# Kernel tuning notes

Hardware: AMD Instinct MI355X
Metric: run time of the kernel (lower is better)

Reference implementation:

```python
import jax, jax.numpy as jnp
import numpy as np

KAPPA = 1.0
SIGMA = 0.3
EPS = 1e-5  # torch BatchNorm1d default eps


def _bn(y, g, b):
    # training-mode batch norm: biased batch statistics over the batch axis
    mu = jnp.mean(y, axis=0)
    var = jnp.mean((y - mu) ** 2, axis=0)
    return g * (y - mu) * jax.lax.rsqrt(var + EPS) + b


def _hid(x, W, b, g, be):
    # Linear -> BatchNorm1d -> ReLU
    return jax.nn.relu(_bn(x @ W + b, g, be))


def setup_inputs() -> dict:
    key = jax.random.key(0)
    ks = jax.random.split(key, 12)
    B, D, H, T = 2048, 256, 266, 51  # H = dim + 10
    S = T - 1
    sc = jnp.float32(0.1)
    f32 = jnp.float32
    inp = {}
    inp["x"] = jax.random.normal(ks[0], (B, D), f32)
    inp["dW"] = jax.random.normal(ks[1], (S, B, D), f32)   # hoisted per-step noise xi
    inp["law"] = jax.random.normal(ks[2], (S, D), f32)
    inp["timegrid"] = jnp.linspace(0.0, 1.0, T).astype(f32)
    # per-timestep MLP stacks (i_h1 / h1_h2 / h2_o)
    inp["W1"] = sc * jax.random.normal(ks[3], (S, D, H), f32)
    inp["b1"] = jnp.zeros((S, H), f32)
    inp["g1"] = jnp.ones((S, H), f32)
    inp["be1"] = jnp.zeros((S, H), f32)
    inp["W2"] = sc * jax.random.normal(ks[4], (S, H, H), f32)
    inp["b2"] = jnp.zeros((S, H), f32)
    inp["g2"] = jnp.ones((S, H), f32)
    inp["be2"] = jnp.zeros((S, H), f32)
    inp["W3"] = sc * jax.random.normal(ks[5], (S, H, D), f32)
    inp["b3"] = jnp.zeros((S, D), f32)
    # v0 network (v0_i_h1 / v0_h1_h2 / v0_h2_o, all Linear+BN+ReLU)
    inp["Wv1"] = sc * jax.random.normal(ks[6], (D, H), f32)
    inp["bv1"] = jnp.zeros((H,), f32)
    inp["gv1"] = jnp.ones((H,), f32)
    inp["bev1"] = jnp.zeros((H,), f32)
    inp["Wv2"] = sc * jax.random.normal(ks[7], (H, H), f32)
    inp["bv2"] = jnp.zeros((H,), f32)
    inp["gv2"] = jnp.ones((H,), f32)
    inp["bev2"] = jnp.zeros((H,), f32)
    inp["Wv3"] = sc * jax.random.normal(ks[8], (H, 1), f32)
    inp["bv3"] = jnp.zeros((1,), f32)
    inp["gv3"] = jnp.ones((1,), f32)
    inp["bev3"] = jnp.zeros((1,), f32)
    return inp


def reference(x, dW, law, timegrid,
              W1, b1, g1, be1, W2, b2, g2, be2, W3, b3,
              Wv1, bv1, gv1, bev1, Wv2, bv2, gv2, bev2, Wv3, bv3, gv3, bev3):
    hgrid = jnp.diff(timegrid)  # [S]
    # v0 network evaluated on the initial state (note: last stage is also Linear+BN+ReLU)
    v0 = _hid(_hid(_hid(x, Wv1, bv1, gv1, bev1), Wv2, bv2, gv2, bev2), Wv3, bv3, gv3, bev3)  # [B,1]

    def step(carry, xs):
        xc, v = carry
        w1, bb1, gg1, bbe1, w2, bb2, gg2, bbe2, w3, bb3, li, dw, h = xs
        h1 = _hid(xc, w1, bb1, gg1, bbe1)
        h2 = _hid(h1, w2, bb2, gg2, bbe2)
        grad = h2 @ w3 + bb3                                   # [B,D]
        # f = kappa^2/2 * ||x - law_i||^2 + 1/2 * ||alpha||^2,  alpha = -grad
        f = 0.5 * KAPPA ** 2 * jnp.sum((xc - li) ** 2, axis=1) + 0.5 * jnp.sum(grad ** 2, axis=1)
        noise = SIGMA * jnp.sqrt(h) * dw                       # [B,D]
        # diag(grad @ noise^T) == rowwise dot product: O(B*D) instead of O(B^2*D)
        v = v - (f * h)[:, None] + jnp.sum(grad * noise, axis=1, keepdims=True)
        xc = xc - grad * h + noise
        return (xc, v), None

    (x_final, v), _ = jax.lax.scan(
        step, (x, v0),
        (W1, b1, g1, be1, W2, b2, g2, be2, W3, b3, law, dW, hgrid))
    return v  # [B,1]; (x_final and the path are byproducts of the same scan)
```

## Files before the change

kernel.cpp:

```cpp
#include <hip/hip_runtime.h>
#include <hip/hip_bf16.h>


#define BATCH 2048
#define DD    256
#define HH    266
#define HP    272
#define SS    50
#define BN_EPS 1e-5f
#define SIG   0.3f
#define AS_STRIDE 296
#define YS    276
#define XS    260

#define V_OFF  1638400
#define S1_OFF 1640448
#define S2_OFF 1649152
#define S1V_OFF 1657856
#define S2V_OFF 1662208
#define SV_OFF  1666560
#define WQ_OFF  1666576

#define W1S 69632
#define W2S 78336
#define W3S 73728
#define W1Q_OFF 0
#define W2Q_OFF 3481600
#define W3Q_OFF 7398400
#define WV1Q_OFF 11084800
#define WV2Q_OFF 11154432

#define BAR_OFF 7283200

typedef unsigned short ushort_t;
using short8 = __attribute__((ext_vector_type(8))) short;
using f32x4  = __attribute__((ext_vector_type(4))) float;
using f32x2  = __attribute__((ext_vector_type(2))) float;

__device__ __forceinline__ ushort_t f2b(float f) {
    unsigned u = __float_as_uint(f);
    unsigned r = u + 0x7FFF + ((u >> 16) & 1);
    return (ushort_t)(r >> 16);
}

__device__ __forceinline__ float ld_coh(const float* p) {
    return __hip_atomic_load((const float*)p, __ATOMIC_RELAXED, __HIP_MEMORY_SCOPE_AGENT);
}
__device__ __forceinline__ f32x2 ld2_coh(const float* p) {
    f32x2 v;
    asm volatile("global_load_dwordx2 %0, %1, off sc0 sc1" : "=v"(v) : "v"(p));
    return v;
}
__device__ __forceinline__ void pf2(const f32x4* q, int n, int tid,
                                    f32x4& r0, f32x4& r1) {
    int i0 = (tid < n) ? tid : 0;
    int i1 = (tid + 512 < n) ? (tid + 512) : 0;
    r0 = q[i0];
    r1 = q[i1];
}

__global__ __launch_bounds__(256) void k_conv(const float* __restrict__ src,
                                              ushort_t* __restrict__ dst,
                                              int K, int N, int KT, int NT,
                                              long total) {
    long t = (long)blockIdx.x * 256 + threadIdx.x;
    if (t >= total) return;
    int per = KT * NT * 512;
    int step = (int)(t / per);
    int e = (int)(t - (long)step * per);
    int kt = e / (NT * 512);
    int r = e - kt * NT * 512;
    int nt = r / 512;
    int r2 = r & 511;
    int lane = r2 >> 3;
    int j = r2 & 7;
    int k = kt * 32 + (lane >> 4) * 8 + j;
    int n = nt * 16 + (lane & 15);
    float v = (k < K && n < N) ? src[(size_t)step * K * N + (size_t)k * N + n] : 0.f;
    dst[t] = f2b(v);
}

__global__ __launch_bounds__(256) void k_pre(float* __restrict__ ws) {
    unsigned* bar = (unsigned*)(ws + BAR_OFF);
    for (int i = threadIdx.x; i < 768; i += 256) atomicExch(bar + i, 0u);
}

__device__ __forceinline__ void grid_bar(unsigned* bar, unsigned gen, int bid) {
    __syncthreads();
    if (threadIdx.x == 0) {
        const int lf = bid & 7;
        unsigned* leaf = bar + lf * 32;
        unsigned* root = bar + 256;
        unsigned* rel  = bar + 288 + lf * 32;
        bool done = false;
        unsigned a = __hip_atomic_fetch_add(leaf, 1u, __ATOMIC_RELAXED, __HIP_MEMORY_SCOPE_AGENT);
        if (a == gen * 16u + 15u) {
            unsigned r = __hip_atomic_fetch_add(root, 1u, __ATOMIC_RELAXED, __HIP_MEMORY_SCOPE_AGENT);
            if (r == gen * 8u + 7u) {
                #pragma unroll
                for (int l = 0; l < 8; ++l)
                    __hip_atomic_store(bar + 288 + l * 32, gen + 1u, __ATOMIC_RELAXED, __HIP_MEMORY_SCOPE_AGENT);
                done = true;
            }
        }
        if (!done) {
            while (__hip_atomic_load(rel, __ATOMIC_RELAXED, __HIP_MEMORY_SCOPE_AGENT) < gen + 1u)
                __builtin_amdgcn_s_sleep(1);
        }
        asm volatile("" ::: "memory");
    }
    __syncthreads();
}

__device__ __forceinline__ void compute_ac_coh(const float* __restrict__ si,
                                               const float* __restrict__ g,
                                               const float* __restrict__ be,
                                               float (*AC)[HP]) {
    int t = threadIdx.x;
    if (t < 136) {
        f32x2 sv[8], qv[8];
        #pragma unroll
        for (int r = 0; r < 8; ++r) {
            sv[r] = ld2_coh(si + r * 544 + 2 * t);
            qv[r] = ld2_coh(si + r * 544 + 272 + 2 * t);
        }
        asm volatile("s_waitcnt vmcnt(0)" ::: "memory");
        __builtin_amdgcn_sched_barrier(0);
        f32x2 s = sv[0], q = qv[0];
        #pragma unroll
        for (int r = 1; r < 8; ++r) { s += sv[r]; q += qv[r]; }
        #pragma unroll
        for (int j = 0; j < 2; ++j) {
            int col = 2 * t + j;
            float a = 0.f, c = 0.f;
            if (col < HH) {
                float mu  = s[j] * (1.0f / 2048.0f);
                float var = q[j] * (1.0f / 2048.0f) - mu * mu;
                float rs  = rsqrtf(fmaxf(var, 0.0f) + BN_EPS);
                a = g[col] * rs;
                c = be[col] - mu * a;
            }
            AC[0][col] = a;
            AC[1][col] = c;
        }
    }
}

__device__ __forceinline__ void dev_lin16(
    int bid, int mode, int KT,
    const float* __restrict__ gsrc, const float* __restrict__ lsrc,
    const float* __restrict__ stats_in, const float* __restrict__ g,
    const float* __restrict__ be,
    const ushort_t* __restrict__ Wq, const float* __restrict__ bias,
    float* __restrict__ ylds, float* __restrict__ stats_out,
    float* __restrict__ zero_ptr,
    ushort_t* __restrict__ As, float (*AC)[HP])
{
    const int tid  = threadIdx.x;
    const int lane = tid & 63;
    const int wv   = tid >> 6;
    const int quad = lane >> 4;
    const int l15  = lane & 15;
    const int row0 = bid * 16;

    if (zero_ptr != nullptr && tid < 34)
        atomicExch(zero_ptr + bid * 34 + tid, 0.0f);

    if (mode == 2) { compute_ac_coh(stats_in, g, be, AC); __syncthreads(); }

    const int PAIRS = KT * 16;
    for (int idx = tid; idx < 16 * PAIRS; idx += 512) {
        int m  = idx / PAIRS;
        int kk = (idx - m * PAIRS) * 2;
        float v0, v1;
        if (mode == 2) {
            v0 = (kk < HH)   ? fmaxf(fmaf(AC[0][kk],   lsrc[m * YS + kk],   AC[1][kk]),   0.f) : 0.f;
            v1 = (kk+1 < HH) ? fmaxf(fmaf(AC[0][kk+1], lsrc[m * YS + kk+1], AC[1][kk+1]), 0.f) : 0.f;
        } else {
            v0 = gsrc[(size_t)(row0 + m) * DD + kk];
            v1 = gsrc[(size_t)(row0 + m) * DD + kk + 1];
        }
        ((unsigned int*)As)[m * (AS_STRIDE/2) + (kk >> 1)] =
            (unsigned int)f2b(v0) | ((unsigned int)f2b(v1) << 16);
    }
    __syncthreads();

    f32x4 acc[3];
    #pragma unroll
    for (int i = 0; i < 3; ++i) acc[i] = (f32x4){0.f, 0.f, 0.f, 0.f};

    #pragma unroll 3
    for (int kt = 0; kt < KT; ++kt) {
        short8 af = *(const short8*)(&As[l15 * AS_STRIDE + kt * 32 + quad * 8]);
        const ushort_t* wp = Wq + ((size_t)(kt * 17 + wv)) * 512 + lane * 8;
        #pragma unroll
        for (int i = 0; i < 3; ++i) {
            if (i < 2 || wv == 0) {
                short8 bf = *(const short8*)(wp + (size_t)i * 8 * 512);
                acc[i] = __builtin_amdgcn_mfma_f32_16x16x32_bf16(af, bf, acc[i], 0, 0, 0);
            }
        }
    }

    #pragma unroll
    for (int i = 0; i < 3; ++i) {
        if (i == 2 && wv != 0) continue;
        int t = wv + 8 * i;
        int col = t * 16 + l15;
        float bj = (col < HH) ? bias[col] : 0.f;
        float y0 = acc[i][0] + bj, y1 = acc[i][1] + bj;
        float y2 = acc[i][2] + bj, y3 = acc[i][3] + bj;
        ylds[(quad*4 + 0) * YS + col] = y0;
        ylds[(quad*4 + 1) * YS + col] = y1;
        ylds[(quad*4 + 2) * YS + col] = y2;
        ylds[(quad*4 + 3) * YS + col] = y3;
        float sp = y0 + y1 + y2 + y3;
        float sq = y0*y0 + y1*y1 + y2*y2 + y3*y3;
        sp += __shfl_xor(sp, 16); sp += __shfl_xor(sp, 32);
        sq += __shfl_xor(sq, 16); sq += __shfl_xor(sq, 32);
        if (quad == 0 && col < HH) {
            float* spp = stats_out + (bid & 7) * 544;
            atomicAdd(spp + col, sp);
            atomicAdd(spp + 272 + col, sq);
        }
    }
}

__device__ __forceinline__ void dev_fused16(
    int bid,
    const float* __restrict__ y2l, const float* __restrict__ stats_in,
    const float* __restrict__ g2, const float* __restrict__ be2,
    const ushort_t* __restrict__ W3q, const float* __restrict__ b3,
    const float* __restrict__ law, const float* __restrict__ dWs,
    const float* __restrict__ tg, int s, int doP1,
    float* __restrict__ xcl, float* __restrict__ vv, float* __restrict__ outv,
    const ushort_t* __restrict__ W1q, const float* __restrict__ b1n,
    float* __restrict__ y1l, float* __restrict__ stats_out,
    float* __restrict__ zero_ptr,
    ushort_t* __restrict__ As, float (*AC)[HP], float* __restrict__ red)
{
    const int tid  = threadIdx.x;
    const int lane = tid & 63;
    const int wv   = tid >> 6;
    const int quad = lane >> 4;
    const int l15  = lane & 15;
    const int row0 = bid * 16;

    if (zero_ptr != nullptr && tid < 34)
        atomicExch(zero_ptr + bid * 34 + tid, 0.0f);

    compute_ac_coh(stats_in, g2, be2, AC);
    __syncthreads();

    for (int idx = tid; idx < 16 * 144; idx += 512) {
        int m  = idx / 144;
        int kk = (idx - m * 144) * 2;
        float v0 = (kk < HH)   ? fmaxf(fmaf(AC[0][kk],   y2l[m * YS + kk],   AC[1][kk]),   0.f) : 0.f;
        float v1 = (kk+1 < HH) ? fmaxf(fmaf(AC[0][kk+1], y2l[m * YS + kk+1], AC[1][kk+1]), 0.f) : 0.f;
        ((unsigned int*)As)[m * (AS_STRIDE/2) + (kk >> 1)] =
            (unsigned int)f2b(v0) | ((unsigned int)f2b(v1) << 16);
    }
    __syncthreads();

    f32x4 acc[2];
    acc[0] = (f32x4){0.f,0.f,0.f,0.f};
    acc[1] = (f32x4){0.f,0.f,0.f,0.f};
    #pragma unroll 3
    for (int kt = 0; kt < 9; ++kt) {
        short8 af = *(const short8*)(&As[l15 * AS_STRIDE + kt * 32 + quad * 8]);
        const ushort_t* wp = W3q + ((size_t)(kt * 16 + wv)) * 512 + lane * 8;
        acc[0] = __builtin_amdgcn_mfma_f32_16x16x32_bf16(af, *(const short8*)(wp),           acc[0], 0, 0, 0);
        acc[1] = __builtin_amdgcn_mfma_f32_16x16x32_bf16(af, *(const short8*)(wp + 8 * 512), acc[1], 0, 0, 0);
    }

    const float h   = tg[s + 1] - tg[s];
    const float srt = SIG * sqrtf(h);
    float grad[2][4], xcv[2][4], dwv[2][4];
    float sxr[4], sgr[4], sgnr[4];
    #pragma unroll
    for (int i = 0; i < 2; ++i) {
        int col = (wv + 8*i) * 16 + l15;
        const float lawv = law[col];
        const float b3v  = b3[col];
        #pragma unroll
        for (int r = 0; r < 4; ++r) {
            int rl = quad * 4 + r;
            float gd = acc[i][r] + b3v;
            float xv = xcl[rl * XS + col];
            float dw = dWs[(size_t)(row0 + rl) * DD + col];
            float d  = xv - lawv;
            grad[i][r] = gd; xcv[i][r] = xv; dwv[i][r] = dw;
            if (i == 0) {
                sxr[r]  = d * d;
                sgr[r]  = gd * gd;
                sgnr[r] = gd * dw;
            } else {
                sxr[r]  = fmaf(d, d, sxr[r]);
                sgr[r]  = fmaf(gd, gd, sgr[r]);
                sgnr[r] = fmaf(gd, dw, sgnr[r]);
            }
        }
    }
    #pragma unroll
    for (int off = 1; off < 16; off <<= 1) {
        #pragma unroll
        for (int r = 0; r < 4; ++r) {
            sxr[r]  += __shfl_xor(sxr[r],  off);
            sgr[r]  += __shfl_xor(sgr[r],  off);
            sgnr[r] += __shfl_xor(sgnr[r], off);
        }
    }
    if (l15 == 0) {
        #pragma unroll
        for (int r = 0; r < 4; ++r) {
            int rr = quad * 4 + r;
            red[(wv * 16 + rr) * 3 + 0] = sxr[r];
            red[(wv * 16 + rr) * 3 + 1] = sgr[r];
            red[(wv * 16 + rr) * 3 + 2] = sgnr[r];
        }
    }
    __syncthreads();

    if (tid < 16) {
        float sx = 0.f, sg = 0.f, sgn = 0.f;
        #pragma unroll
        for (int w = 0; w < 8; ++w) {
            sx  += red[(w * 16 + tid) * 3 + 0];
            sg  += red[(w * 16 + tid) * 3 + 1];
            sgn += red[(w * 16 + tid) * 3 + 2];
        }
        int row = row0 + tid;
        float f  = 0.5f * (sx + sg);
        float vn = vv[row] - f * h + srt * sgn;
        vv[row] = vn;
        if (s == SS - 1) outv[row] = vn;
    }

    #pragma unroll
    for (int i = 0; i < 2; ++i) {
        int col = (wv + 8*i) * 16 + l15;
        #pragma unroll
        for (int r = 0; r < 4; ++r) {
            int rl = quad * 4 + r;
            float xn = xcv[i][r] - grad[i][r] * h + srt * dwv[i][r];
            xcl[rl * XS + col] = xn;
            if (doP1) As[rl * AS_STRIDE + col] = f2b(xn);
        }
    }
    if (!doP1) return;
    __syncthreads();

    f32x4 acc2[3];
    #pragma unroll
    for (int i = 0; i < 3; ++i) acc2[i] = (f32x4){0.f, 0.f, 0.f, 0.f};
    #pragma unroll 4
    for (int kt = 0; kt < 8; ++kt) {
        short8 af = *(const short8*)(&As[l15 * AS_STRIDE + kt * 32 + quad * 8]);
        const ushort_t* wp = W1q + ((size_t)(kt * 17 + wv)) * 512 + lane * 8;
        #pragma unroll
        for (int i = 0; i < 3; ++i) {
            if (i < 2 || wv == 0) {
                short8 bf = *(const short8*)(wp + (size_t)i * 8 * 512);
                acc2[i] = __builtin_amdgcn_mfma_f32_16x16x32_bf16(af, bf, acc2[i], 0, 0, 0);
            }
        }
    }
    #pragma unroll
    for (int i = 0; i < 3; ++i) {
        if (i == 2 && wv != 0) continue;
        int t = wv + 8 * i;
        int col = t * 16 + l15;
        float bj = (col < HH) ? b1n[col] : 0.f;
        float y0 = acc2[i][0] + bj, y1 = acc2[i][1] + bj;
        float y2 = acc2[i][2] + bj, y3 = acc2[i][3] + bj;
        y1l[(quad*4 + 0) * YS + col] = y0;
        y1l[(quad*4 + 1) * YS + col] = y1;
        y1l[(quad*4 + 2) * YS + col] = y2;
        y1l[(quad*4 + 3) * YS + col] = y3;
        float sp = y0 + y1 + y2 + y3;
        float sq = y0*y0 + y1*y1 + y2*y2 + y3*y3;
        sp += __shfl_xor(sp, 16); sp += __shfl_xor(sp, 32);
        sq += __shfl_xor(sq, 16); sq += __shfl_xor(sq, 32);
        if (quad == 0 && col < HH) {
            float* spp = stats_out + (bid & 7) * 544;
            atomicAdd(spp + col, sp);
            atomicAdd(spp + 272 + col, sq);
        }
    }
}

__device__ __forceinline__ void dev_v0l3_16(
    int bid, const float* __restrict__ y2l, const float* __restrict__ stats_in,
    const float* __restrict__ gv, const float* __restrict__ bev,
    const float* __restrict__ wv3, const float* __restrict__ bv3,
    float* __restrict__ vout, float* __restrict__ sv,
    float (*AC)[HP], float* __restrict__ xtra)
{
    const int tid = threadIdx.x;
    compute_ac_coh(stats_in, gv, bev, AC);
    __syncthreads();

    const int r  = tid >> 5;
    const int ks = tid & 31;
    int k0 = ks * 9, k1 = k0 + 9;
    if (k1 > HH) k1 = HH;
    float acc = 0.0f;
    for (int k = k0; k < k1; ++k) {
        float y  = y2l[r * YS + k];
        float a2 = fmaxf(fmaf(AC[0][k], y, AC[1][k]), 0.0f);
        acc = fmaf(a2, wv3[k], acc);
    }
    #pragma unroll
    for (int off = 1; off < 32; off <<= 1) acc += __shfl_xor(acc, off);
    if (ks == 0) {
        float y = acc + bv3[0];
        vout[bid * 16 + r] = y;
        xtra[r] = y;
        xtra[16 + r] = y * y;
    }
    __syncthreads();
    if (tid == 0) {
        float s = 0.f, q = 0.f;
        #pragma unroll
        for (int i = 0; i < 16; ++i) { s += xtra[i]; q += xtra[16 + i]; }
        atomicAdd(sv, s);
        atomicAdd(sv + 1, q);
    }
}

__device__ __forceinline__ void dev_v0fin16(int bid, float* __restrict__ v,
                                            const float* __restrict__ sv,
                                            const float* __restrict__ gv3,
                                            const float* __restrict__ bev3) {
    if (threadIdx.x < 16) {
        float s0 = ld_coh(sv);
        float s1 = ld_coh(sv + 1);
        float mu  = s0 * (1.0f / 2048.0f);
        float var = s1 * (1.0f / 2048.0f) - mu * mu;
        float rs  = rsqrtf(fmaxf(var, 0.0f) + BN_EPS);
        int row = bid * 16 + threadIdx.x;
        float y = v[row];
        v[row] = fmaxf(gv3[0] * (y - mu) * rs + bev3[0], 0.0f);
    }
}

__global__ __launch_bounds__(512) void k_persist(
    const float* __restrict__ x, const float* __restrict__ dW,
    const float* __restrict__ law, const float* __restrict__ tg,
    const float* __restrict__ b1, const float* __restrict__ g1, const float* __restrict__ be1,
    const float* __restrict__ b2, const float* __restrict__ g2, const float* __restrict__ be2,
    const float* __restrict__ b3,
    const float* __restrict__ bv1, const float* __restrict__ gv1, const float* __restrict__ bev1,
    const float* __restrict__ bv2, const float* __restrict__ gv2, const float* __restrict__ bev2,
    const float* __restrict__ Wv3, const float* __restrict__ bv3,
    const float* __restrict__ gv3, const float* __restrict__ bev3,
    float* __restrict__ ws, float* __restrict__ out)
{
    __shared__ ushort_t As[16 * AS_STRIDE];
    __shared__ float AC[2][HP];
    __shared__ float Y1s[16 * YS];
    __shared__ float Y2s[16 * YS];
    __shared__ float XCs[16 * XS];
    __shared__ float XTRA[384];

    const int bid = blockIdx.x;
    const int tid = threadIdx.x;

    float* V   = ws + V_OFF;
    float* S1  = ws + S1_OFF;
    float* S2  = ws + S2_OFF;
    float* S1v = ws + S1V_OFF;
    float* S2v = ws + S2V_OFF;
    float* SV  = ws + SV_OFF;
    ushort_t* WQ = (ushort_t*)(ws + WQ_OFF);
    ushort_t* W1q  = WQ + W1Q_OFF;
    ushort_t* W2q  = WQ + W2Q_OFF;
    ushort_t* W3q  = WQ + W3Q_OFF;
    ushort_t* Wv1q = WQ + WV1Q_OFF;
    ushort_t* Wv2q = WQ + WV2Q_OFF;
    unsigned* bar  = (unsigned*)(ws + BAR_OFF);

    unsigned gen = 0;
    const int sl = (bid >> 3) & 15;

    for (int i = tid; i < 16 * DD; i += 512) {
        int r = i >> 8, c = i & 255;
        XCs[r * XS + c] = x[(size_t)bid * 16 * DD + i];
    }
    {
        int z = bid * 205 + tid;
        int ze = (bid + 1) * 205; if (ze > 26128) ze = 26128;
        if (tid < 205 && z < ze) atomicExch(S1 + z, 0.0f);
    }
    grid_bar(bar, gen, bid); gen++;

    dev_lin16(bid, 0, 8, x, nullptr, nullptr, nullptr, nullptr,
              Wv1q, bv1, Y1s, S1v, nullptr, As, AC);
    grid_bar(bar, gen, bid); gen++;

    dev_lin16(bid, 2, 9, nullptr, Y1s, S1v, gv1, bev1,
              Wv2q, bv2, Y2s, S2v, nullptr, As, AC);
    grid_bar(bar, gen, bid); gen++;

    dev_v0l3_16(bid, Y2s, S2v, gv2, bev2, Wv3, bv3, V, SV, AC, XTRA);
    grid_bar(bar, gen, bid); gen++;

    dev_v0fin16(bid, V, SV, gv3, bev3);
    dev_lin16(bid, 0, 8, x, nullptr, nullptr, nullptr, nullptr,
              W1q, b1, Y1s, S1, nullptr, As, AC);
    {
        f32x4 p0, p1;
        pf2((const f32x4*)((const char*)W2q + (size_t)sl * 9792), 612, tid, p0, p1);
        asm volatile("" :: "v"(p0), "v"(p1));
    }
    grid_bar(bar, gen, bid); gen++;

    for (int s = 0; s < SS; ++s) {
        int p = s & 1;
        dev_lin16(bid, 2, 9, nullptr, Y1s, S1 + p * 4352,
                  g1 + s * HH, be1 + s * HH,
                  W2q + (size_t)s * W2S, b2 + s * HH,
                  Y2s, S2 + p * 4352, S1 + (1 - p) * 4352, As, AC);
        {
            f32x4 d0, d1, w30, w31, w10, w11, lb;
            pf2((const f32x4*)(dW + (size_t)s * BATCH * DD + (size_t)bid * 16 * DD),
                1024, tid, d0, d1);
            pf2((const f32x4*)((const char*)(W3q + (size_t)s * W3S) + (size_t)sl * 9216),
                576, tid, w30, w31);
            int sn0 = (s + 1 < SS) ? s + 1 : s;
            pf2((const f32x4*)((const char*)(W1q + (size_t)sn0 * W1S) + (size_t)sl * 8704),
                544, tid, w10, w11);
            const f32x4* ql = (const f32x4*)(law + (size_t)s * DD);
            const f32x4* qb = (const f32x4*)(b3 + (size_t)s * DD);
            lb = (tid < 64) ? ql[tid] : ((tid < 128) ? qb[tid - 64] : ql[0]);
            asm volatile("" :: "v"(d0), "v"(d1), "v"(w30), "v"(w31),
                              "v"(w10), "v"(w11), "v"(lb));
        }
        grid_bar(bar, gen, bid); gen++;

        int sn = (s + 1 < SS) ? s + 1 : 0;
        dev_fused16(bid, Y2s, S2 + p * 4352,
                    g2 + s * HH, be2 + s * HH,
                    W3q + (size_t)s * W3S, b3 + s * DD,
                    law + s * DD, dW + (size_t)s * BATCH * DD,
                    tg, s, (s < SS - 1) ? 1 : 0,
                    XCs, V, out,
                    W1q + (size_t)sn * W1S, b1 + sn * HH,
                    Y1s, S1 + ((s + 1) & 1) * 4352,
                    S2 + (1 - p) * 4352, As, AC, XTRA);
        if (s + 1 < SS) {
            f32x4 p0, p1;
            pf2((const f32x4*)((const char*)(W2q + (size_t)(s + 1) * W2S) + (size_t)sl * 9792),
                612, tid, p0, p1);
            asm volatile("" :: "v"(p0), "v"(p1));
        }
        grid_bar(bar, gen, bid); gen++;
    }
}

extern "C" void kernel_launch(void* const* d_in, const int* in_sizes, int n_in,
                              void* d_out, int out_size, void* d_ws, size_t ws_size,
                              hipStream_t stream)
{
    (void)in_sizes; (void)n_in; (void)out_size; (void)ws_size;
    const float* x    = (const float*)d_in[0];
    const float* dW   = (const float*)d_in[1];
    const float* law  = (const float*)d_in[2];
    const float* tg   = (const float*)d_in[3];
    const float* W1   = (const float*)d_in[4];
    const float* b1   = (const float*)d_in[5];
    const float* g1   = (const float*)d_in[6];
    const float* be1  = (const float*)d_in[7];
    const float* W2   = (const float*)d_in[8];
    const float* b2   = (const float*)d_in[9];
    const float* g2   = (const float*)d_in[10];
    const float* be2  = (const float*)d_in[11];
    const float* W3   = (const float*)d_in[12];
    const float* b3   = (const float*)d_in[13];
    const float* Wv1  = (const float*)d_in[14];
    const float* bv1  = (const float*)d_in[15];
    const float* gv1  = (const float*)d_in[16];
    const float* bev1 = (const float*)d_in[17];
    const float* Wv2  = (const float*)d_in[18];
    const float* bv2  = (const float*)d_in[19];
    const float* gv2  = (const float*)d_in[20];
    const float* bev2 = (const float*)d_in[21];
    const float* Wv3  = (const float*)d_in[22];
    const float* bv3  = (const float*)d_in[23];
    const float* gv3  = (const float*)d_in[24];
    const float* bev3 = (const float*)d_in[25];

    float* ws = (float*)d_ws;
    ushort_t* WQ = (ushort_t*)(ws + WQ_OFF);
    ushort_t* W1q  = WQ + W1Q_OFF;
    ushort_t* W2q  = WQ + W2Q_OFF;
    ushort_t* W3q  = WQ + W3Q_OFF;
    ushort_t* Wv1q = WQ + WV1Q_OFF;
    ushort_t* Wv2q = WQ + WV2Q_OFF;
    float* out = (float*)d_out;

    k_pre<<<1, 256, 0, stream>>>(ws);
    k_conv<<<13600, 256, 0, stream>>>(W1,  W1q,  DD, HH, 8, 17, (long)SS * W1S);
    k_conv<<<15300, 256, 0, stream>>>(W2,  W2q,  HH, HH, 9, 17, (long)SS * W2S);
    k_conv<<<14400, 256, 0, stream>>>(W3,  W3q,  HH, DD, 9, 16, (long)SS * W3S);
    k_conv<<<272,   256, 0, stream>>>(Wv1, Wv1q, DD, HH, 8, 17, (long)W1S);
    k_conv<<<306,   256, 0, stream>>>(Wv2, Wv2q, HH, HH, 9, 17, (long)W2S);

    k_persist<<<128, 512, 0, stream>>>(
        x, dW, law, tg,
        b1, g1, be1, b2, g2, be2, b3,
        bv1, gv1, bev1, bv2, gv2, bev2,
        Wv3, bv3, gv3, bev3,
        ws, out);
}
```

Before: 1.233 ms.

## Build MFMA A-fragments in registers instead of staging bf16 tiles in LDS

Drops the LDS staging pass that converted activations (with BN+ReLU applied) to bf16 in a shared tile and then synchronized. Each lane now builds its A fragment inside the MFMA k-loop, reading fp32 values from LDS or global and applying the BN affine transform, ReLU and bf16 rounding in registers. In the third-layer/update routine, the dW, law and b3 loads are also moved to the start so their latency overlaps the stats computation. This removes a barrier and a write/read round trip per layer, but every wave now redoes the same conversion and reads twice the bytes as fp32.

Result: slower. 1.285 ms (+4.2%).

```diff
diff --git a/kernel.cpp b/kernel.cpp
--- a/kernel.cpp
+++ b/kernel.cpp
@@ -41,6 +41,34 @@
     unsigned u = __float_as_uint(f);
     unsigned r = u + 0x7FFF + ((u >> 16) & 1);
     return (ushort_t)(r >> 16);
+}
+__device__ __forceinline__ short8 mk_af(const float* __restrict__ yp,
+                                        const float* __restrict__ a0,
+                                        const float* __restrict__ c0) {
+    unsigned u[4];
+    #pragma unroll
+    for (int j = 0; j < 4; ++j) {
+        float r0 = fmaxf(fmaf(a0[2*j],   yp[2*j],   c0[2*j]),   0.f);
+        float r1 = fmaxf(fmaf(a0[2*j+1], yp[2*j+1], c0[2*j+1]), 0.f);
+        u[j] = (unsigned)f2b(r0) | ((unsigned)f2b(r1) << 16);
+    }
+    union { unsigned q[4]; short8 s; } cv;
+    cv.q[0]=u[0]; cv.q[1]=u[1]; cv.q[2]=u[2]; cv.q[3]=u[3];
+    return cv.s;
+}
+__device__ __forceinline__ short8 mk_raw(const float* __restrict__ xp) {
+    unsigned u[4];
+    #pragma unroll
+    for (int j = 0; j < 4; ++j)
+        u[j] = (unsigned)f2b(xp[2*j]) | ((unsigned)f2b(xp[2*j+1]) << 16);
+    union { unsigned q[4]; short8 s; } cv;
+    cv.q[0]=u[0]; cv.q[1]=u[1]; cv.q[2]=u[2]; cv.q[3]=u[3];
+    return cv.s;
+}
+__device__ __forceinline__ short8 zero8() {
+    union { unsigned q[4]; short8 s; } cv;
+    cv.q[0]=0; cv.q[1]=0; cv.q[2]=0; cv.q[3]=0;
+    return cv.s;
 }
 
 __device__ __forceinline__ float ld_coh(const float* p) {
@@ -153,8 +181,7 @@
     const float* __restrict__ be,
     const ushort_t* __restrict__ Wq, const float* __restrict__ bias,
     float* __restrict__ ylds, float* __restrict__ stats_out,
-    float* __restrict__ zero_ptr,
-    ushort_t* __restrict__ As, float (*AC)[HP])
+    float* __restrict__ zero_ptr, float (*AC)[HP])
 {
     const int tid  = threadIdx.x;
     const int lane = tid & 63;
@@ -168,22 +195,8 @@
 
     if (mode == 2) { compute_ac_coh(stats_in, g, be, AC); __syncthreads(); }
 
-    const int PAIRS = KT * 16;
-    for (int idx = tid; idx < 16 * PAIRS; idx += 512) {
-        int m  = idx / PAIRS;
-        int kk = (idx - m * PAIRS) * 2;
-        float v0, v1;
-        if (mode == 2) {
-            v0 = (kk < HH)   ? fmaxf(fmaf(AC[0][kk],   lsrc[m * YS + kk],   AC[1][kk]),   0.f) : 0.f;
-            v1 = (kk+1 < HH) ? fmaxf(fmaf(AC[0][kk+1], lsrc[m * YS + kk+1], AC[1][kk+1]), 0.f) : 0.f;
-        } else {
-            v0 = gsrc[(size_t)(row0 + m) * DD + kk];
-            v1 = gsrc[(size_t)(row0 + m) * DD + kk + 1];
-        }
-        ((unsigned int*)As)[m * (AS_STRIDE/2) + (kk >> 1)] =
-            (unsigned int)f2b(v0) | ((unsigned int)f2b(v1) << 16);
-    }
-    __syncthreads();
+    const float* yrow = (mode == 2) ? (lsrc + l15 * YS)
+                                    : (gsrc + (size_t)(row0 + l15) * DD);
 
     f32x4 acc[3];
     #pragma unroll
@@ -191,7 +204,11 @@
 
     #pragma unroll 3
     for (int kt = 0; kt < KT; ++kt) {
-        short8 af = *(const short8*)(&As[l15 * AS_STRIDE + kt * 32 + quad * 8]);
+        int k0 = kt * 32 + quad * 8;
+        short8 af;
+        if (mode == 0)       af = mk_raw(yrow + k0);
+        else if (k0 < HP)    af = mk_af(yrow + k0, &AC[0][k0], &AC[1][k0]);
+        else                 af = zero8();
         const ushort_t* wp = Wq + ((size_t)(kt * 17 + wv)) * 512 + lane * 8;
         #pragma unroll
         for (int i = 0; i < 3; ++i) {
@@ -245,6 +262,18 @@
     const int quad = lane >> 4;
     const int l15  = lane & 15;
     const int row0 = bid * 16;
+    const int col0 = wv * 16 + l15;
+    const int col1 = (wv + 8) * 16 + l15;
+
+    float dwv[2][4], lawv[2], b3v[2];
+    #pragma unroll
+    for (int r = 0; r < 4; ++r) {
+        int rowg = row0 + quad * 4 + r;
+        dwv[0][r] = dWs[(size_t)rowg * DD + col0];
+        dwv[1][r] = dWs[(size_t)rowg * DD + col1];
+    }
+    lawv[0] = law[col0]; lawv[1] = law[col1];
+    b3v[0]  = b3[col0];  b3v[1]  = b3[col1];
 
     if (zero_ptr != nullptr && tid < 34)
         atomicExch(zero_ptr + bid * 34 + tid, 0.0f);
@@ -252,22 +281,14 @@
     compute_ac_coh(stats_in, g2, be2, AC);
     __syncthreads();
 
-    for (int idx = tid; idx < 16 * 144; idx += 512) {
-        int m  = idx / 144;
-        int kk = (idx - m * 144) * 2;
-        float v0 = (kk < HH)   ? fmaxf(fmaf(AC[0][kk],   y2l[m * YS + kk],   AC[1][kk]),   0.f) : 0.f;
-        float v1 = (kk+1 < HH) ? fmaxf(fmaf(AC[0][kk+1], y2l[m * YS + kk+1], AC[1][kk+1]), 0.f) : 0.f;
-        ((unsigned int*)As)[m * (AS_STRIDE/2) + (kk >> 1)] =
-            (unsigned int)f2b(v0) | ((unsigned int)f2b(v1) << 16);
-    }
-    __syncthreads();
-
+    const float* yrow = y2l + l15 * YS;
     f32x4 acc[2];
     acc[0] = (f32x4){0.f,0.f,0.f,0.f};
     acc[1] = (f32x4){0.f,0.f,0.f,0.f};
     #pragma unroll 3
     for (int kt = 0; kt < 9; ++kt) {
-        short8 af = *(const short8*)(&As[l15 * AS_STRIDE + kt * 32 + quad * 8]);
+        int k0 = kt * 32 + quad * 8;
+        short8 af = (k0 < HP) ? mk_af(yrow + k0, &AC[0][k0], &AC[1][k0]) : zero8();
         const ushort_t* wp = W3q + ((size_t)(kt * 16 + wv)) * 512 + lane * 8;
         acc[0] = __builtin_amdgcn_mfma_f32_16x16x32_bf16(af, *(const short8*)(wp),           acc[0], 0, 0, 0);
         acc[1] = __builtin_amdgcn_mfma_f32_16x16x32_bf16(af, *(const short8*)(wp + 8 * 512), acc[1], 0, 0, 0);
@@ -275,21 +296,19 @@
 
     const float h   = tg[s + 1] - tg[s];
     const float srt = SIG * sqrtf(h);
-    float grad[2][4], xcv[2][4], dwv[2][4];
+    float grad[2][4], xcv[2][4];
     float sxr[4], sgr[4], sgnr[4];
     #pragma unroll
     for (int i = 0; i < 2; ++i) {
-        int col = (wv + 8*i) * 16 + l15;
-        const float lawv = law[col];
-        const float b3v  = b3[col];
+        int col = (i == 0) ? col0 : col1;
         #pragma unroll
         for (int r = 0; r < 4; ++r) {
             int rl = quad * 4 + r;
-            float gd = acc[i][r] + b3v;
+            float gd = acc[i][r] + b3v[i];
             float xv = xcl[rl * XS + col];
-            float dw = dWs[(size_t)(row0 + rl) * DD + col];
-            float d  = xv - lawv;
-            grad[i][r] = gd; xcv[i][r] = xv; dwv[i][r] = dw;
+            float dw = dwv[i][r];
+            float d  = xv - lawv[i];
+            grad[i][r] = gd; xcv[i][r] = xv;
             if (i == 0) {
                 sxr[r]  = d * d;
                 sgr[r]  = gd * gd;
@@ -338,7 +357,7 @@
 
     #pragma unroll
     for (int i = 0; i < 2; ++i) {
-        int col = (wv + 8*i) * 16 + l15;
+        int col = (i == 0) ? col0 : col1;
         #pragma unroll
         for (int r = 0; r < 4; ++r) {
             int rl = quad * 4 + r;
@@ -495,11 +514,11 @@
     grid_bar(bar, gen, bid); gen++;
 
     dev_lin16(bid, 0, 8, x, nullptr, nullptr, nullptr, nullptr,
-              Wv1q, bv1, Y1s, S1v, nullptr, As, AC);
+              Wv1q, bv1, Y1s, S1v, nullptr, AC);
     grid_bar(bar, gen, bid); gen++;
 
     dev_lin16(bid, 2, 9, nullptr, Y1s, S1v, gv1, bev1,
-              Wv2q, bv2, Y2s, S2v, nullptr, As, AC);
+              Wv2q, bv2, Y2s, S2v, nullptr, AC);
     grid_bar(bar, gen, bid); gen++;
 
     dev_v0l3_16(bid, Y2s, S2v, gv2, bev2, Wv3, bv3, V, SV, AC, XTRA);
@@ -507,7 +526,7 @@
 
     dev_v0fin16(bid, V, SV, gv3, bev3);
     dev_lin16(bid, 0, 8, x, nullptr, nullptr, nullptr, nullptr,
-              W1q, b1, Y1s, S1, nullptr, As, AC);
+              W1q, b1, Y1s, S1, nullptr, AC);
     {
         f32x4 p0, p1;
         pf2((const f32x4*)((const char*)W2q + (size_t)sl * 9792), 612, tid, p0, p1);
@@ -520,7 +539,7 @@
         dev_lin16(bid, 2, 9, nullptr, Y1s, S1 + p * 4352,
                   g1 + s * HH, be1 + s * HH,
                   W2q + (size_t)s * W2S, b2 + s * HH,
-                  Y2s, S2 + p * 4352, S1 + (1 - p) * 4352, As, AC);
+                  Y2s, S2 + p * 4352, S1 + (1 - p) * 4352, AC);
         {
             f32x4 d0, d1, w30, w31, w10, w11, lb;
             pf2((const f32x4*)(dW + (size_t)s * BATCH * DD + (size_t)bid * 16 * DD),
```
